# Kernel optimization log

Measured on AMD Instinct MI355X. Metric: run time of the kernel, lower is better.

Reference implementation:

```python
import jax, jax.numpy as jnp
import numpy as np

N_NODES, N_EDGES, N_FEAT, N_GRAPHS = 100_000, 1_600_000, 3, 512
FENG = jnp.array([4, 8, 9, 12, 13, 14])  # feng_filters(): second-order pairs with scale2 > scale1
LEAKY_SLOPE = 0.01


def _wavelet_constructor():
    # Psi_j = P^{2^{j-1}} - P^{2^j}, j = 1..4, over 17 diffusion levels P^0..P^16
    W = np.zeros((4, 17), dtype=np.float32)
    for j, (a, b) in enumerate([(1, 2), (2, 4), (4, 8), (8, 16)]):
        W[j, a] = 1.0
        W[j, b] = -1.0
    return jnp.asarray(W)


def _gcn_edges(edge_index, n):
    # gcn_norm with self-loops: w_ij = d_i^-1/2 d_j^-1/2 on A + I
    loop = jnp.arange(n)
    src = jnp.concatenate([edge_index[0], loop])
    dst = jnp.concatenate([edge_index[1], loop])
    deg = jax.ops.segment_sum(jnp.ones_like(dst, dtype=jnp.float32), dst, num_segments=n)
    dinv = jnp.where(deg > 0, jax.lax.rsqrt(deg), 0.0)
    w = dinv[src] * dinv[dst]
    return src, dst, w


def _diffuse(x, src, dst, w, n):
    # lazy random walk: 0.5 * (x + P_norm x), x: [N, C, k]
    agg = jax.ops.segment_sum(w[:, None, None] * x[src], dst, num_segments=n)
    return 0.5 * (x + agg)


def _scatter_features(x, edge_index):
    n, c = x.shape
    src, dst, w = _gcn_edges(edge_index, n)
    Wav = _wavelet_constructor()

    s0 = x[:, :, None]                                   # [N, C, 1]
    levels = [s0]
    for _ in range(16):
        levels.append(_diffuse(levels[-1], src, dst, w, n))
    D = jnp.stack(levels)                                # [17, N, C, 1]
    sub = jnp.einsum('wt,tnck->wnck', Wav, D)[..., 0]    # [4, N, C]
    s1 = jnp.abs(jnp.transpose(sub, (1, 2, 0)))          # [N, C, 4]

    levels2 = [s1]
    for _ in range(16):
        levels2.append(_diffuse(levels2[-1], src, dst, w, n))
    D2 = jnp.stack(levels2)                              # [17, N, C, 4]
    sub2 = jnp.einsum('wt,tncf->wncf', Wav, D2)          # [4, N, C, 4]
    # reproduce the exact torch transpose/reshape sequence of LEGS Scatter
    t = jnp.abs(jnp.transpose(sub2, (1, 0, 2, 3)).reshape(n, c, 16))  # [N, C, 16]
    s2 = jnp.swapaxes(t, 1, 2)[:, FENG]                  # [N, 6, C]

    xcat = jnp.concatenate([s0, s1], axis=2)             # [N, C, 5]
    xcat = jnp.swapaxes(xcat, 1, 2)                      # [N, 5, C]
    xcat = jnp.concatenate([xcat, s2], axis=1)           # [N, 11, C]
    return xcat.reshape(n, 11 * c)                       # [N, 33]


def _scatter_moments(x, batch, num_graphs):
    # per-graph mean / variance / skew (3 central moments), concatenated -> [G, 3*F]
    cnt = jax.ops.segment_sum(jnp.ones((x.shape[0],), x.dtype), batch, num_segments=num_graphs)
    cnt = jnp.maximum(cnt, 1.0)[:, None]
    mean = jax.ops.segment_sum(x, batch, num_segments=num_graphs) / cnt
    dev = x - mean[batch]
    var = jax.ops.segment_sum(dev * dev, batch, num_segments=num_graphs) / cnt
    skew = jax.ops.segment_sum(dev * dev * dev, batch, num_segments=num_graphs) / cnt
    return jnp.concatenate([mean, var, skew], axis=1)


def setup_inputs() -> dict:
    key = jax.random.key(0)
    ks = jax.random.split(key, 8)
    x = jax.random.normal(ks[0], (N_NODES, N_FEAT), dtype=jnp.float32)
    edge_index = jax.random.randint(ks[1], (2, N_EDGES), 0, N_NODES)
    batch = jnp.sort(jax.random.randint(ks[2], (N_NODES,), 0, N_GRAPHS))

    def lin(k, fan_in, fan_out):
        k1, k2 = jax.random.split(k)
        bound = 1.0 / np.sqrt(fan_in)
        W = jax.random.uniform(k1, (fan_in, fan_out), minval=-bound, maxval=bound, dtype=jnp.float32)
        b = jax.random.uniform(k2, (fan_out,), minval=-bound, maxval=bound, dtype=jnp.float32)
        return W, b

    W1, b1 = lin(ks[3], 99, 128)
    W2, b2 = lin(ks[4], 128, 64)
    W3, b3 = lin(ks[5], 64, 64)
    We, be = lin(ks[6], 64, 32)
    Wc, bc = lin(ks[7], 32, 1)
    return {"x": x, "W1": W1, "b1": b1, "W2": W2, "b2": b2, "W3": W3, "b3": b3,
            "We": We, "be": be, "Wc": Wc, "bc": bc,
            "edge_index": edge_index, "batch": batch, "num_graphs": N_GRAPHS}


def reference(x, W1, b1, W2, b2, W3, b3, We, be, Wc, bc, edge_index, batch, num_graphs):
    act = lambda v: jax.nn.leaky_relu(v, LEAKY_SLOPE)
    feats = _scatter_features(x, edge_index)              # [N, 33]
    h = _scatter_moments(feats, batch, num_graphs)        # [G, 99]
    h = act(h)
    h = act(h @ W1 + b1)        # dropout is identity (p=0.0)
    h = act(h @ W2 + b2)
    h = h @ W3 + b3             # no activation before embedding layer (as in source)
    embedding = h @ We + be
    output = embedding @ Wc + bc  # classifier applied to embedding (pre-activation)
    return embedding, output
```

## Files before the change

### kernel.cpp

```cpp
#include <hip/hip_runtime.h>

#define N_NODES 100000
#define N_EDGES 1600000
#define NG      512
#define NPART   8
#define NPP     12500
#define BCAP    245760
#define BQ      1024
#define BFLUSH  512
#define NBBLK   256
#define EPB     ((N_EDGES + NBBLK - 1) / NBBLK)
#define SCAT_SLICES 128

static __device__ __forceinline__ float lrelu(float v) {
    return v >= 0.0f ? v : 0.01f * v;
}

__global__ void k_zero_i32(int* __restrict__ p, int n) {
    int i = blockIdx.x * blockDim.x + threadIdx.x;
    if (i < n) p[i] = 0;
}

__global__ void k_copy_i32(const int* __restrict__ s, int* __restrict__ d, int n) {
    int i = blockIdx.x * blockDim.x + threadIdx.x;
    if (i < n) d[i] = s[i];
}

__global__ void k_dinv(const int* __restrict__ counts, float* __restrict__ dinv,
                       float* __restrict__ dinv2, float* __restrict__ sdeg) {
    int i = blockIdx.x * blockDim.x + threadIdx.x;
    if (i < N_NODES) {
        float deg = (float)(counts[i] + 1);
        float s = sqrtf(deg);
        sdeg[i] = s;
        dinv[i] = 1.0f / s;
        dinv2[i] = 1.0f / deg;
    }
}

__global__ __launch_bounds__(256) void k_bin(const int* __restrict__ esrc,
                                             const int* __restrict__ edst,
                                             int* __restrict__ gcur,
                                             uint2* __restrict__ gbuf) {
    __shared__ uint2 buf[NPART][BQ];
    __shared__ int lcnt[NPART];
    __shared__ int gbase[NPART];
    if (threadIdx.x < NPART) lcnt[threadIdx.x] = 0;
    __syncthreads();
    int base = blockIdx.x * EPB;
    int end = base + EPB; if (end > N_EDGES) end = N_EDGES;
    for (int r = base; r < end; r += 2048) {
        int rend = r + 2048; if (rend > end) rend = end;
        for (int e = r + (int)threadIdx.x; e < rend; e += 256) {
            int d = edst[e];
            int s = esrc[e];
            int b = d / NPP;
            int pos = atomicAdd(&lcnt[b], 1);
            if (pos < BQ) {
                buf[b][pos] = make_uint2((unsigned)s, (unsigned)d);
            } else {
                int g = atomicAdd(&gcur[b], 1);
                gbuf[(size_t)b * BCAP + g] = make_uint2((unsigned)s, (unsigned)d);
            }
        }
        __syncthreads();
        for (int b = 0; b < NPART; ++b) {
            int cnt = lcnt[b];
            if (cnt >= BFLUSH) {
                if (threadIdx.x == 0) gbase[b] = atomicAdd(&gcur[b], BFLUSH);
                __syncthreads();
                int gb = gbase[b];
                for (int i = threadIdx.x; i < BFLUSH; i += 256)
                    gbuf[(size_t)b * BCAP + gb + i] = buf[b][i];
                __syncthreads();
                int inb = cnt < BQ ? cnt : BQ;
                int rem = inb - BFLUSH;
                for (int i = threadIdx.x; i < rem; i += 256)
                    buf[b][i] = buf[b][BFLUSH + i];
                __syncthreads();
                if (threadIdx.x == 0) lcnt[b] = rem;
                __syncthreads();
            }
        }
    }
    for (int b = 0; b < NPART; ++b) {
        int cnt = lcnt[b]; if (cnt > BQ) cnt = BQ;
        if (cnt > 0) {
            if (threadIdx.x == 0) gbase[b] = atomicAdd(&gcur[b], cnt);
            __syncthreads();
            int gb = gbase[b];
            for (int i = threadIdx.x; i < cnt; i += 256)
                gbuf[(size_t)b * BCAP + gb + i] = buf[b][i];
        }
        __syncthreads();
    }
}

__global__ __launch_bounds__(1024) void k_count_b(const int* __restrict__ gcur,
                                                  const uint2* __restrict__ gbuf,
                                                  int* __restrict__ counts) {
    __shared__ int h[NPP];
    int p = blockIdx.x & (NPART - 1);
    int slice = blockIdx.x >> 3;
    for (int i = threadIdx.x; i < NPP; i += 1024) h[i] = 0;
    __syncthreads();
    int n = gcur[p];
    int per = (n + 7) / 8;
    int lo = slice * per, hi = lo + per; if (hi > n) hi = n;
    const uint2* bb = gbuf + (size_t)p * BCAP;
    int pl = p * NPP;
    for (int i = lo + (int)threadIdx.x; i < hi; i += 1024) {
        int d = (int)bb[i].y - pl;
        atomicAdd(&h[d], 1);
    }
    __syncthreads();
    for (int i = threadIdx.x; i < NPP; i += 1024)
        if (h[i]) atomicAdd(&counts[pl + i], h[i]);
}

__global__ void k_scan_block(const int* __restrict__ counts, int* __restrict__ offsets,
                             int* __restrict__ bsums, int n) {
    __shared__ int tmp[1024];
    int gid = blockIdx.x * 1024 + threadIdx.x;
    int v = (gid < n) ? counts[gid] : 0;
    tmp[threadIdx.x] = v;
    __syncthreads();
    for (int off = 1; off < 1024; off <<= 1) {
        int t = (threadIdx.x >= off) ? tmp[threadIdx.x - off] : 0;
        __syncthreads();
        tmp[threadIdx.x] += t;
        __syncthreads();
    }
    if (gid < n) offsets[gid + 1] = tmp[threadIdx.x];
    if (threadIdx.x == 1023) bsums[blockIdx.x] = tmp[1023];
}

__global__ void k_scan_bsums(int* __restrict__ bsums, int nb) {
    if (blockIdx.x == 0 && threadIdx.x == 0) {
        int acc = 0;
        for (int b = 0; b < nb; ++b) { int v = bsums[b]; bsums[b] = acc; acc += v; }
    }
}

__global__ void k_scan_add(int* __restrict__ offsets, const int* __restrict__ bsums, int n) {
    int gid = blockIdx.x * 1024 + threadIdx.x;
    if (gid < n) offsets[gid + 1] += bsums[blockIdx.x];
    if (gid == 0) offsets[0] = 0;
}

__global__ __launch_bounds__(256) void k_scatter_b(const int* __restrict__ gcur,
                                                   const uint2* __restrict__ gbuf,
                                                   int* __restrict__ cursor,
                                                   int* __restrict__ csr_src) {
    int p = blockIdx.x & (NPART - 1);
    int slice = blockIdx.x >> 3;
    int n = gcur[p];
    int per = (n + SCAT_SLICES - 1) / SCAT_SLICES;
    int lo = slice * per, hi = lo + per; if (hi > n) hi = n;
    const uint2* bb = gbuf + (size_t)p * BCAP;
    for (int i = lo + (int)threadIdx.x; i < hi; i += 256) {
        uint2 e = bb[i];
        int pos = atomicAdd(&cursor[e.y], 1);
        csr_src[pos] = (int)e.x;
    }
}

__global__ void k_vinit(const float* __restrict__ x, const float* __restrict__ dinv,
                        float4* __restrict__ v) {
    int i = blockIdx.x * blockDim.x + threadIdx.x;
    if (i >= N_NODES) return;
    float di = dinv[i];
    v[i] = make_float4(di * x[i * 3 + 0], di * x[i * 3 + 1], di * x[i * 3 + 2], 0.0f);
}

__global__ __launch_bounds__(256) void k_vdiff3(
    const float4* __restrict__ xin, float4* __restrict__ xout,
    const int* __restrict__ offs, const int* __restrict__ csrc,
    const float* __restrict__ dinv2) {
    int t = blockIdx.x * 256 + threadIdx.x;
    if (t >= N_NODES * 8) return;
    int h = t & 7;
    int i = t >> 3;
    int b = offs[i], e = offs[i + 1];
    float a0 = 0.0f, a1 = 0.0f, a2 = 0.0f;
    for (int p = b + h; p < e; p += 8) {
        int s = csrc[p];
        float4 xv = xin[s];
        a0 += xv.x; a1 += xv.y; a2 += xv.z;
    }
    a0 += __shfl_xor(a0, 1, 64); a1 += __shfl_xor(a1, 1, 64); a2 += __shfl_xor(a2, 1, 64);
    a0 += __shfl_xor(a0, 2, 64); a1 += __shfl_xor(a1, 2, 64); a2 += __shfl_xor(a2, 2, 64);
    a0 += __shfl_xor(a0, 4, 64); a1 += __shfl_xor(a1, 4, 64); a2 += __shfl_xor(a2, 4, 64);
    if (h == 0) {
        float d2 = dinv2[i];
        float4 sv = xin[i];
        xout[i] = make_float4(0.5f * (sv.x + d2 * (a0 + sv.x)),
                              0.5f * (sv.y + d2 * (a1 + sv.y)),
                              0.5f * (sv.z + d2 * (a2 + sv.z)), 0.0f);
    }
}

__global__ __launch_bounds__(256) void k_vdiff12(
    const float4* __restrict__ xin, float4* __restrict__ xout,
    const int* __restrict__ offs, const int* __restrict__ csrc,
    const float* __restrict__ dinv2) {
    int t = blockIdx.x * 256 + threadIdx.x;
    if (t >= N_NODES * 8) return;
    int h = t & 7;
    int i = t >> 3;
    int b = offs[i], e = offs[i + 1];
    float a[12];
#pragma unroll
    for (int c = 0; c < 12; ++c) a[c] = 0.0f;
    for (int p = b + h; p < e; p += 8) {
        int s = csrc[p];
        float4 b0 = xin[s * 3 + 0];
        float4 b1 = xin[s * 3 + 1];
        float4 b2 = xin[s * 3 + 2];
        a[0] += b0.x; a[1] += b0.y; a[2]  += b0.z; a[3]  += b0.w;
        a[4] += b1.x; a[5] += b1.y; a[6]  += b1.z; a[7]  += b1.w;
        a[8] += b2.x; a[9] += b2.y; a[10] += b2.z; a[11] += b2.w;
    }
#pragma unroll
    for (int c = 0; c < 12; ++c) {
        a[c] += __shfl_xor(a[c], 1, 64);
        a[c] += __shfl_xor(a[c], 2, 64);
        a[c] += __shfl_xor(a[c], 4, 64);
    }
    if (h == 0) {
        float d2 = dinv2[i];
        float4 s0 = xin[i * 3 + 0], s1 = xin[i * 3 + 1], s2 = xin[i * 3 + 2];
        xout[i * 3 + 0] = make_float4(0.5f * (s0.x + d2 * (a[0] + s0.x)),
                                      0.5f * (s0.y + d2 * (a[1] + s0.y)),
                                      0.5f * (s0.z + d2 * (a[2] + s0.z)),
                                      0.5f * (s0.w + d2 * (a[3] + s0.w)));
        xout[i * 3 + 1] = make_float4(0.5f * (s1.x + d2 * (a[4] + s1.x)),
                                      0.5f * (s1.y + d2 * (a[5] + s1.y)),
                                      0.5f * (s1.z + d2 * (a[6] + s1.z)),
                                      0.5f * (s1.w + d2 * (a[7] + s1.w)));
        xout[i * 3 + 2] = make_float4(0.5f * (s2.x + d2 * (a[8] + s2.x)),
                                      0.5f * (s2.y + d2 * (a[9] + s2.y)),
                                      0.5f * (s2.z + d2 * (a[10] + s2.z)),
                                      0.5f * (s2.w + d2 * (a[11] + s2.w)));
    }
}

__global__ void k_s1v(const float4* __restrict__ L1, const float4* __restrict__ L2,
                      const float4* __restrict__ L4, const float4* __restrict__ L8,
                      const float4* __restrict__ L16, float* __restrict__ s1v) {
    int i = blockIdx.x * blockDim.x + threadIdx.x;
    if (i >= N_NODES) return;
    float4 v[5];
    v[0] = L1[i]; v[1] = L2[i]; v[2] = L4[i]; v[3] = L8[i]; v[4] = L16[i];
    float* out = s1v + (size_t)i * 12;
#pragma unroll
    for (int f = 0; f < 4; ++f) {
        out[0 * 4 + f] = fabsf(v[f].x - v[f + 1].x);
        out[1 * 4 + f] = fabsf(v[f].y - v[f + 1].y);
        out[2 * 4 + f] = fabsf(v[f].z - v[f + 1].z);
    }
}

__global__ void k_feats(const float* __restrict__ x, const float* __restrict__ s1v,
                        const float* __restrict__ M1, const float* __restrict__ M2,
                        const float* __restrict__ M4, const float* __restrict__ M8,
                        const float* __restrict__ M16, const float* __restrict__ sdeg,
                        float* __restrict__ feats) {
    int i = blockIdx.x * blockDim.x + threadIdx.x;
    if (i >= N_NODES) return;
    float sd = sdeg[i];
    float* out = feats + (size_t)i * 33;
    out[0] = x[i * 3 + 0];
    out[1] = x[i * 3 + 1];
    out[2] = x[i * 3 + 2];
    for (int r = 1; r <= 4; ++r)
        for (int c = 0; c < 3; ++c)
            out[r * 3 + c] = sd * s1v[(size_t)i * 12 + c * 4 + (r - 1)];
    const float* Ms[5] = {M1, M2, M4, M8, M16};
    const int FENG[6] = {4, 8, 9, 12, 13, 14};
    for (int m = 0; m < 6; ++m) {
        for (int c2 = 0; c2 < 3; ++c2) {
            int idx = c2 * 16 + FENG[m];
            int w = idx / 12, rem = idx % 12, cc = rem / 4, f = rem % 4;
            float v = Ms[w][(size_t)i * 12 + cc * 4 + f] - Ms[w + 1][(size_t)i * 12 + cc * 4 + f];
            out[(5 + m) * 3 + c2] = fabsf(sd * v);
        }
    }
}

static __device__ __forceinline__ int lower_bound_i(const int* __restrict__ a, int n, int key) {
    int lo = 0, hi = n;
    while (lo < hi) { int mid = (lo + hi) >> 1; if (a[mid] < key) lo = mid + 1; else hi = mid; }
    return lo;
}

__global__ __launch_bounds__(256) void k_moments(
    const float* __restrict__ feats, const int* __restrict__ batch,
    float* __restrict__ h0) {
    __shared__ float P1[4][33], P2[4][33], P3[4][33];
    int g = blockIdx.x;
    int lo = lower_bound_i(batch, N_NODES, g);
    int hi = lower_bound_i(batch, N_NODES, g + 1);
    int w = threadIdx.x >> 6;
    int l = threadIdx.x & 63;
    float s1 = 0.0f, s2 = 0.0f, s3 = 0.0f;
    if (l < 33) {
        for (int i = lo + w; i < hi; i += 4) {
            float v = feats[(size_t)i * 33 + l];
            s1 += v;
            s2 += v * v;
            s3 += v * v * v;
        }
        P1[w][l] = s1; P2[w][l] = s2; P3[w][l] = s3;
    }
    __syncthreads();
    if (threadIdx.x < 33) {
        int c = threadIdx.x;
        float S1 = P1[0][c] + P1[1][c] + P1[2][c] + P1[3][c];
        float S2 = P2[0][c] + P2[1][c] + P2[2][c] + P2[3][c];
        float S3 = P3[0][c] + P3[1][c] + P3[2][c] + P3[3][c];
        float cnt = (float)((hi - lo) > 1 ? (hi - lo) : 1);
        float mu  = S1 / cnt;
        float ex2 = S2 / cnt;
        float ex3 = S3 / cnt;
        float var = ex2 - mu * mu;
        float skw = ex3 - 3.0f * mu * ex2 + 2.0f * mu * mu * mu;
        h0[g * 99 + c]      = lrelu(mu);
        h0[g * 99 + 33 + c] = lrelu(var);
        h0[g * 99 + 66 + c] = lrelu(skw);
    }
}

__global__ __launch_bounds__(128) void k_mlp(
    const float* __restrict__ h0,
    const float* __restrict__ W1, const float* __restrict__ b1,
    const float* __restrict__ W2, const float* __restrict__ b2,
    const float* __restrict__ W3, const float* __restrict__ b3,
    const float* __restrict__ We, const float* __restrict__ be,
    const float* __restrict__ Wc, const float* __restrict__ bc,
    float* __restrict__ emb, float* __restrict__ outp) {
    __shared__ float s0[99], s1[128], s2[64], s3[64], s4[32];
    int g = blockIdx.x;
    int t = threadIdx.x;
    if (t < 99) s0[t] = h0[g * 99 + t];
    __syncthreads();
    {
        float a = b1[t];
        for (int k = 0; k < 99; ++k) a += s0[k] * W1[k * 128 + t];
        s1[t] = lrelu(a);
    }
    __syncthreads();
    if (t < 64) {
        float a = b2[t];
        for (int k = 0; k < 128; ++k) a += s1[k] * W2[k * 64 + t];
        s2[t] = lrelu(a);
    }
    __syncthreads();
    if (t < 64) {
        float a = b3[t];
        for (int k = 0; k < 64; ++k) a += s2[k] * W3[k * 64 + t];
        s3[t] = a;
    }
    __syncthreads();
    if (t < 32) {
        float a = be[t];
        for (int k = 0; k < 64; ++k) a += s3[k] * We[k * 32 + t];
        s4[t] = a;
        emb[g * 32 + t] = a;
    }
    __syncthreads();
    if (t == 0) {
        float a = bc[0];
        for (int k = 0; k < 32; ++k) a += s4[k] * Wc[k];
        outp[g] = a;
    }
}

extern "C" void kernel_launch(void* const* d_in, const int* in_sizes, int n_in,
                              void* d_out, int out_size, void* d_ws, size_t ws_size,
                              hipStream_t stream) {
    const float* x   = (const float*)d_in[0];
    const float* W1  = (const float*)d_in[1];
    const float* b1  = (const float*)d_in[2];
    const float* W2  = (const float*)d_in[3];
    const float* b2  = (const float*)d_in[4];
    const float* W3  = (const float*)d_in[5];
    const float* b3  = (const float*)d_in[6];
    const float* We  = (const float*)d_in[7];
    const float* be  = (const float*)d_in[8];
    const float* Wc  = (const float*)d_in[9];
    const float* bc  = (const float*)d_in[10];
    const int*   eix = (const int*)d_in[11];
    const int*   batch = (const int*)d_in[12];
    const int* esrc = eix;
    const int* edst = eix + N_EDGES;

    char* ws = (char*)d_ws;
    size_t off = 0;
    auto alloc = [&](size_t bytes) -> void* {
        void* p = ws + off;
        off = (off + bytes + 255) & ~(size_t)255;
        return p;
    };
    int*   counts  = (int*)alloc((size_t)N_NODES * 4);
    int*   offsets = (int*)alloc((size_t)(N_NODES + 1) * 4);
    int*   cursor  = (int*)alloc((size_t)N_NODES * 4);
    float* dinv    = (float*)alloc((size_t)N_NODES * 4);
    float* dinv2   = (float*)alloc((size_t)N_NODES * 4);
    float* sdeg    = (float*)alloc((size_t)N_NODES * 4);
    int*   bsums   = (int*)alloc(1024 * 4);
    int*   gcur    = (int*)alloc(NPART * 4);
    uint2* gbuf    = (uint2*)alloc((size_t)NPART * BCAP * 8);
    int*   csr_src = (int*)alloc((size_t)N_EDGES * 4);
    float4* v0     = (float4*)alloc((size_t)N_NODES * 16);
    float4* p1[7];
    for (int i = 0; i < 7; ++i) p1[i] = (float4*)alloc((size_t)N_NODES * 16);
    float* s1v = (float*)alloc((size_t)N_NODES * 12 * 4);
    float* p2[7];
    for (int i = 0; i < 7; ++i) p2[i] = (float*)alloc((size_t)N_NODES * 12 * 4);
    float* feats = (float*)alloc((size_t)N_NODES * 33 * 4);
    float* h0 = (float*)alloc((size_t)NG * 99 * 4);
    (void)ws_size; (void)in_sizes; (void)n_in; (void)out_size;

    const int TB = 256;
    const int gbN = (N_NODES + TB - 1) / TB;
    const int nbScan = (N_NODES + 1023) / 1024;

    hipLaunchKernelGGL(k_zero_i32, dim3(gbN), dim3(TB), 0, stream, counts, N_NODES);
    hipLaunchKernelGGL(k_zero_i32, dim3(1), dim3(TB), 0, stream, gcur, NPART);
    hipLaunchKernelGGL(k_bin, dim3(NBBLK), dim3(TB), 0, stream, esrc, edst, gcur, gbuf);
    hipLaunchKernelGGL(k_count_b, dim3(64), dim3(1024), 0, stream, gcur, gbuf, counts);
    hipLaunchKernelGGL(k_dinv, dim3(gbN), dim3(TB), 0, stream, counts, dinv, dinv2, sdeg);
    hipLaunchKernelGGL(k_scan_block, dim3(nbScan), dim3(1024), 0, stream, counts, offsets, bsums, N_NODES);
    hipLaunchKernelGGL(k_scan_bsums, dim3(1), dim3(1), 0, stream, bsums, nbScan);
    hipLaunchKernelGGL(k_scan_add, dim3(nbScan), dim3(1024), 0, stream, offsets, bsums, N_NODES);
    hipLaunchKernelGGL(k_copy_i32, dim3(gbN), dim3(TB), 0, stream, offsets, cursor, N_NODES);
    hipLaunchKernelGGL(k_scatter_b, dim3(NPART * SCAT_SLICES), dim3(TB), 0, stream,
                       gcur, gbuf, cursor, csr_src);

    hipLaunchKernelGGL(k_vinit, dim3(gbN), dim3(TB), 0, stream, x, dinv, v0);

    const int saveT[5] = {1, 2, 4, 8, 16};

    const float4* prev = v0;
    float4* saves1[5];
    {
        int si = 0, sc = 0;
        const int gb = (N_NODES * 8 + TB - 1) / TB;
        for (int t = 1; t <= 16; ++t) {
            float4* outb;
            if (si < 5 && t == saveT[si]) { outb = p1[si]; saves1[si] = outb; ++si; }
            else { outb = p1[5 + sc]; sc ^= 1; }
            hipLaunchKernelGGL(k_vdiff3, dim3(gb), dim3(TB), 0, stream,
                               prev, outb, offsets, csr_src, dinv2);
            prev = outb;
        }
    }
    hipLaunchKernelGGL(k_s1v, dim3(gbN), dim3(TB), 0, stream,
                       saves1[0], saves1[1], saves1[2], saves1[3], saves1[4], s1v);

    float* saves2[5];
    {
        const float* prev2 = s1v;
        int si = 0, sc = 0;
        const int gb = (N_NODES * 8 + TB - 1) / TB;
        for (int t = 1; t <= 16; ++t) {
            float* outb;
            if (si < 5 && t == saveT[si]) { outb = p2[si]; saves2[si] = outb; ++si; }
            else { outb = p2[5 + sc]; sc ^= 1; }
            hipLaunchKernelGGL(k_vdiff12, dim3(gb), dim3(TB), 0, stream,
                               (const float4*)prev2, (float4*)outb, offsets, csr_src, dinv2);
            prev2 = outb;
        }
    }

    hipLaunchKernelGGL(k_feats, dim3(gbN), dim3(TB), 0, stream,
                       x, s1v, saves2[0], saves2[1], saves2[2], saves2[3], saves2[4], sdeg, feats);
    hipLaunchKernelGGL(k_moments, dim3(NG), dim3(256), 0, stream, feats, batch, h0);

    float* emb  = (float*)d_out;
    float* outp = (float*)d_out + NG * 32;
    hipLaunchKernelGGL(k_mlp, dim3(NG), dim3(128), 0, stream,
                       h0, W1, b1, W2, b2, W3, b3, We, be, Wc, bc, emb, outp);
}
```

Before: 809.4 us.

## Bin edges into 1024-node sub-ranges and pad second-order features to 16 floats

Replaces the 8-partition edge binning, global-atomic count and global-cursor scatter with 98 fine-grained bins of 1024 destination nodes. Each bin is then counted and placed into CSR with shared-memory histograms and cursors, staging the output in LDS. This removes the separate zero and copy passes and the global atomics on per-node cursors. Separately, the 12-float per-node vectors in the second-order diffusion are padded to 16 floats so each node's gather is 64-byte aligned. The cost is extra memory traffic for the padding and less parallelism during placement, since only 98 blocks run.

```diff
diff --git a/kernel.cpp b/kernel.cpp
--- a/kernel.cpp
+++ b/kernel.cpp
@@ -3,14 +3,13 @@
 #define N_NODES 100000
 #define N_EDGES 1600000
 #define NG      512
-#define NPART   8
-#define NPP     12500
-#define BCAP    245760
-#define BQ      1024
-#define BFLUSH  512
-#define NBBLK   256
-#define EPB     ((N_EDGES + NBBLK - 1) / NBBLK)
-#define SCAT_SLICES 128
+#define NSB     98
+#define SUBR    1024
+#define SCAP    20480
+#define SD      96
+#define B2BLK   256
+#define B2E     ((N_EDGES + B2BLK - 1) / B2BLK)
+#define PCAP    18432
 
 static __device__ __forceinline__ float lrelu(float v) {
     return v >= 0.0f ? v : 0.01f * v;
@@ -19,11 +18,6 @@
 __global__ void k_zero_i32(int* __restrict__ p, int n) {
     int i = blockIdx.x * blockDim.x + threadIdx.x;
     if (i < n) p[i] = 0;
-}
-
-__global__ void k_copy_i32(const int* __restrict__ s, int* __restrict__ d, int n) {
-    int i = blockIdx.x * blockDim.x + threadIdx.x;
-    if (i < n) d[i] = s[i];
 }
 
 __global__ void k_dinv(const int* __restrict__ counts, float* __restrict__ dinv,
@@ -38,84 +32,59 @@
     }
 }
 
-__global__ __launch_bounds__(256) void k_bin(const int* __restrict__ esrc,
-                                             const int* __restrict__ edst,
-                                             int* __restrict__ gcur,
-                                             uint2* __restrict__ gbuf) {
-    __shared__ uint2 buf[NPART][BQ];
-    __shared__ int lcnt[NPART];
-    __shared__ int gbase[NPART];
-    if (threadIdx.x < NPART) lcnt[threadIdx.x] = 0;
-    __syncthreads();
-    int base = blockIdx.x * EPB;
-    int end = base + EPB; if (end > N_EDGES) end = N_EDGES;
-    for (int r = base; r < end; r += 2048) {
-        int rend = r + 2048; if (rend > end) rend = end;
-        for (int e = r + (int)threadIdx.x; e < rend; e += 256) {
-            int d = edst[e];
-            int s = esrc[e];
-            int b = d / NPP;
-            int pos = atomicAdd(&lcnt[b], 1);
-            if (pos < BQ) {
-                buf[b][pos] = make_uint2((unsigned)s, (unsigned)d);
-            } else {
-                int g = atomicAdd(&gcur[b], 1);
-                gbuf[(size_t)b * BCAP + g] = make_uint2((unsigned)s, (unsigned)d);
-            }
+__global__ __launch_bounds__(256) void k_bin2(const int* __restrict__ esrc,
+                                              const int* __restrict__ edst,
+                                              int* __restrict__ gcur,
+                                              uint2* __restrict__ gbuf) {
+    __shared__ uint2 st[NSB][SD];
+    __shared__ int lcnt[NSB];
+    __shared__ int gbase[NSB];
+    for (int i = threadIdx.x; i < NSB; i += 256) lcnt[i] = 0;
+    __syncthreads();
+    int base = blockIdx.x * B2E;
+    int end = base + B2E; if (end > N_EDGES) end = N_EDGES;
+    for (int e = base + (int)threadIdx.x; e < end; e += 256) {
+        int d = edst[e];
+        int s = esrc[e];
+        int b = d >> 10;
+        int pos = atomicAdd(&lcnt[b], 1);
+        if (pos < SD) {
+            st[b][pos] = make_uint2((unsigned)s, (unsigned)d);
+        } else {
+            int g = atomicAdd(&gcur[b], 1);
+            gbuf[(size_t)b * SCAP + g] = make_uint2((unsigned)s, (unsigned)d);
         }
-        __syncthreads();
-        for (int b = 0; b < NPART; ++b) {
-            int cnt = lcnt[b];
-            if (cnt >= BFLUSH) {
-                if (threadIdx.x == 0) gbase[b] = atomicAdd(&gcur[b], BFLUSH);
-                __syncthreads();
-                int gb = gbase[b];
-                for (int i = threadIdx.x; i < BFLUSH; i += 256)
-                    gbuf[(size_t)b * BCAP + gb + i] = buf[b][i];
-                __syncthreads();
-                int inb = cnt < BQ ? cnt : BQ;
-                int rem = inb - BFLUSH;
-                for (int i = threadIdx.x; i < rem; i += 256)
-                    buf[b][i] = buf[b][BFLUSH + i];
-                __syncthreads();
-                if (threadIdx.x == 0) lcnt[b] = rem;
-                __syncthreads();
-            }
-        }
-    }
-    for (int b = 0; b < NPART; ++b) {
-        int cnt = lcnt[b]; if (cnt > BQ) cnt = BQ;
-        if (cnt > 0) {
-            if (threadIdx.x == 0) gbase[b] = atomicAdd(&gcur[b], cnt);
-            __syncthreads();
-            int gb = gbase[b];
-            for (int i = threadIdx.x; i < cnt; i += 256)
-                gbuf[(size_t)b * BCAP + gb + i] = buf[b][i];
-        }
-        __syncthreads();
-    }
-}
-
-__global__ __launch_bounds__(1024) void k_count_b(const int* __restrict__ gcur,
-                                                  const uint2* __restrict__ gbuf,
-                                                  int* __restrict__ counts) {
-    __shared__ int h[NPP];
-    int p = blockIdx.x & (NPART - 1);
-    int slice = blockIdx.x >> 3;
-    for (int i = threadIdx.x; i < NPP; i += 1024) h[i] = 0;
-    __syncthreads();
-    int n = gcur[p];
-    int per = (n + 7) / 8;
-    int lo = slice * per, hi = lo + per; if (hi > n) hi = n;
-    const uint2* bb = gbuf + (size_t)p * BCAP;
-    int pl = p * NPP;
-    for (int i = lo + (int)threadIdx.x; i < hi; i += 1024) {
-        int d = (int)bb[i].y - pl;
-        atomicAdd(&h[d], 1);
-    }
-    __syncthreads();
-    for (int i = threadIdx.x; i < NPP; i += 1024)
-        if (h[i]) atomicAdd(&counts[pl + i], h[i]);
+    }
+    __syncthreads();
+    if (threadIdx.x < NSB) {
+        int c = lcnt[threadIdx.x]; if (c > SD) c = SD;
+        gbase[threadIdx.x] = atomicAdd(&gcur[threadIdx.x], c);
+    }
+    __syncthreads();
+    for (int b = 0; b < NSB; ++b) {
+        int cnt = lcnt[b]; if (cnt > SD) cnt = SD;
+        int gb = gbase[b];
+        for (int i = threadIdx.x; i < cnt; i += 256)
+            gbuf[(size_t)b * SCAP + gb + i] = st[b][i];
+    }
+}
+
+__global__ __launch_bounds__(256) void k_count_s(const int* __restrict__ gcur,
+                                                 const uint2* __restrict__ gbuf,
+                                                 int* __restrict__ counts) {
+    __shared__ int h[SUBR];
+    int sb = blockIdx.x;
+    int lo = sb * SUBR;
+    int nr = N_NODES - lo; if (nr > SUBR) nr = SUBR;
+    for (int i = threadIdx.x; i < nr; i += 256) h[i] = 0;
+    __syncthreads();
+    int n = gcur[sb];
+    const uint2* bb = gbuf + (size_t)sb * SCAP;
+    for (int i = threadIdx.x; i < n; i += 256)
+        atomicAdd(&h[(int)bb[i].y - lo], 1);
+    __syncthreads();
+    for (int i = threadIdx.x; i < nr; i += 256)
+        counts[lo + i] = h[i];
 }
 
 __global__ void k_scan_block(const int* __restrict__ counts, int* __restrict__ offsets,
@@ -148,21 +117,32 @@
     if (gid == 0) offsets[0] = 0;
 }
 
-__global__ __launch_bounds__(256) void k_scatter_b(const int* __restrict__ gcur,
-                                                   const uint2* __restrict__ gbuf,
-                                                   int* __restrict__ cursor,
-                                                   int* __restrict__ csr_src) {
-    int p = blockIdx.x & (NPART - 1);
-    int slice = blockIdx.x >> 3;
-    int n = gcur[p];
-    int per = (n + SCAT_SLICES - 1) / SCAT_SLICES;
-    int lo = slice * per, hi = lo + per; if (hi > n) hi = n;
-    const uint2* bb = gbuf + (size_t)p * BCAP;
-    for (int i = lo + (int)threadIdx.x; i < hi; i += 256) {
+__global__ __launch_bounds__(256) void k_place(const int* __restrict__ gcur,
+                                               const uint2* __restrict__ gbuf,
+                                               const int* __restrict__ offsets,
+                                               int* __restrict__ csr_src) {
+    __shared__ int cur[SUBR];
+    __shared__ int stage[PCAP];
+    int sb = blockIdx.x;
+    int lo = sb * SUBR;
+    int nr = N_NODES - lo; if (nr > SUBR) nr = SUBR;
+    int base = offsets[lo];
+    int total = offsets[lo + nr] - base;
+    for (int i = threadIdx.x; i < nr; i += 256)
+        cur[i] = offsets[lo + i] - base;
+    __syncthreads();
+    int n = gcur[sb];
+    const uint2* bb = gbuf + (size_t)sb * SCAP;
+    for (int i = threadIdx.x; i < n; i += 256) {
         uint2 e = bb[i];
-        int pos = atomicAdd(&cursor[e.y], 1);
-        csr_src[pos] = (int)e.x;
-    }
+        int p = atomicAdd(&cur[(int)e.y - lo], 1);
+        if (p < PCAP) stage[p] = (int)e.x;
+        else csr_src[base + p] = (int)e.x;
+    }
+    __syncthreads();
+    int wtot = total < PCAP ? total : PCAP;
+    for (int i = threadIdx.x; i < wtot; i += 256)
+        csr_src[base + i] = stage[i];
 }
 
 __global__ void k_vinit(const float* __restrict__ x, const float* __restrict__ dinv,
@@ -214,9 +194,9 @@
     for (int c = 0; c < 12; ++c) a[c] = 0.0f;
     for (int p = b + h; p < e; p += 8) {
         int s = csrc[p];
-        float4 b0 = xin[s * 3 + 0];
-        float4 b1 = xin[s * 3 + 1];
-        float4 b2 = xin[s * 3 + 2];
+        float4 b0 = xin[s * 4 + 0];
+        float4 b1 = xin[s * 4 + 1];
+        float4 b2 = xin[s * 4 + 2];
         a[0] += b0.x; a[1] += b0.y; a[2]  += b0.z; a[3]  += b0.w;
         a[4] += b1.x; a[5] += b1.y; a[6]  += b1.z; a[7]  += b1.w;
         a[8] += b2.x; a[9] += b2.y; a[10] += b2.z; a[11] += b2.w;
@@ -229,16 +209,16 @@
     }
     if (h == 0) {
         float d2 = dinv2[i];
-        float4 s0 = xin[i * 3 + 0], s1 = xin[i * 3 + 1], s2 = xin[i * 3 + 2];
-        xout[i * 3 + 0] = make_float4(0.5f * (s0.x + d2 * (a[0] + s0.x)),
+        float4 s0 = xin[i * 4 + 0], s1 = xin[i * 4 + 1], s2 = xin[i * 4 + 2];
+        xout[i * 4 + 0] = make_float4(0.5f * (s0.x + d2 * (a[0] + s0.x)),
                                       0.5f * (s0.y + d2 * (a[1] + s0.y)),
                                       0.5f * (s0.z + d2 * (a[2] + s0.z)),
                                       0.5f * (s0.w + d2 * (a[3] + s0.w)));
-        xout[i * 3 + 1] = make_float4(0.5f * (s1.x + d2 * (a[4] + s1.x)),
+        xout[i * 4 + 1] = make_float4(0.5f * (s1.x + d2 * (a[4] + s1.x)),
                                       0.5f * (s1.y + d2 * (a[5] + s1.y)),
                                       0.5f * (s1.z + d2 * (a[6] + s1.z)),
                                       0.5f * (s1.w + d2 * (a[7] + s1.w)));
-        xout[i * 3 + 2] = make_float4(0.5f * (s2.x + d2 * (a[8] + s2.x)),
+        xout[i * 4 + 2] = make_float4(0.5f * (s2.x + d2 * (a[8] + s2.x)),
                                       0.5f * (s2.y + d2 * (a[9] + s2.y)),
                                       0.5f * (s2.z + d2 * (a[10] + s2.z)),
                                       0.5f * (s2.w + d2 * (a[11] + s2.w)));
@@ -247,12 +227,12 @@
 
 __global__ void k_s1v(const float4* __restrict__ L1, const float4* __restrict__ L2,
                       const float4* __restrict__ L4, const float4* __restrict__ L8,
-                      const float4* __restrict__ L16, float* __restrict__ s1v) {
+                      const float4* __restrict__ L16, float* __restrict__ s1vp) {
     int i = blockIdx.x * blockDim.x + threadIdx.x;
     if (i >= N_NODES) return;
     float4 v[5];
     v[0] = L1[i]; v[1] = L2[i]; v[2] = L4[i]; v[3] = L8[i]; v[4] = L16[i];
-    float* out = s1v + (size_t)i * 12;
+    float* out = s1vp + (size_t)i * 16;
 #pragma unroll
     for (int f = 0; f < 4; ++f) {
         out[0 * 4 + f] = fabsf(v[f].x - v[f + 1].x);
@@ -261,7 +241,7 @@
     }
 }
 
-__global__ void k_feats(const float* __restrict__ x, const float* __restrict__ s1v,
+__global__ void k_feats(const float* __restrict__ x, const float* __restrict__ s1vp,
                         const float* __restrict__ M1, const float* __restrict__ M2,
                         const float* __restrict__ M4, const float* __restrict__ M8,
                         const float* __restrict__ M16, const float* __restrict__ sdeg,
@@ -275,14 +255,14 @@
     out[2] = x[i * 3 + 2];
     for (int r = 1; r <= 4; ++r)
         for (int c = 0; c < 3; ++c)
-            out[r * 3 + c] = sd * s1v[(size_t)i * 12 + c * 4 + (r - 1)];
+            out[r * 3 + c] = sd * s1vp[(size_t)i * 16 + c * 4 + (r - 1)];
     const float* Ms[5] = {M1, M2, M4, M8, M16};
     const int FENG[6] = {4, 8, 9, 12, 13, 14};
     for (int m = 0; m < 6; ++m) {
         for (int c2 = 0; c2 < 3; ++c2) {
             int idx = c2 * 16 + FENG[m];
             int w = idx / 12, rem = idx % 12, cc = rem / 4, f = rem % 4;
-            float v = Ms[w][(size_t)i * 12 + cc * 4 + f] - Ms[w + 1][(size_t)i * 12 + cc * 4 + f];
+            float v = Ms[w][(size_t)i * 16 + cc * 4 + f] - Ms[w + 1][(size_t)i * 16 + cc * 4 + f];
             out[(5 + m) * 3 + c2] = fabsf(sd * v);
         }
     }
@@ -404,20 +384,19 @@
     };
     int*   counts  = (int*)alloc((size_t)N_NODES * 4);
     int*   offsets = (int*)alloc((size_t)(N_NODES + 1) * 4);
-    int*   cursor  = (int*)alloc((size_t)N_NODES * 4);
     float* dinv    = (float*)alloc((size_t)N_NODES * 4);
     float* dinv2   = (float*)alloc((size_t)N_NODES * 4);
     float* sdeg    = (float*)alloc((size_t)N_NODES * 4);
     int*   bsums   = (int*)alloc(1024 * 4);
-    int*   gcur    = (int*)alloc(NPART * 4);
-    uint2* gbuf    = (uint2*)alloc((size_t)NPART * BCAP * 8);
+    int*   gcur    = (int*)alloc(NSB * 4);
+    uint2* gbuf    = (uint2*)alloc((size_t)NSB * SCAP * 8);
     int*   csr_src = (int*)alloc((size_t)N_EDGES * 4);
     float4* v0     = (float4*)alloc((size_t)N_NODES * 16);
     float4* p1[7];
     for (int i = 0; i < 7; ++i) p1[i] = (float4*)alloc((size_t)N_NODES * 16);
-    float* s1v = (float*)alloc((size_t)N_NODES * 12 * 4);
+    float* s1vp = (float*)alloc((size_t)N_NODES * 16 * 4);
     float* p2[7];
-    for (int i = 0; i < 7; ++i) p2[i] = (float*)alloc((size_t)N_NODES * 12 * 4);
+    for (int i = 0; i < 7; ++i) p2[i] = (float*)alloc((size_t)N_NODES * 16 * 4);
     float* feats = (float*)alloc((size_t)N_NODES * 33 * 4);
     float* h0 = (float*)alloc((size_t)NG * 99 * 4);
     (void)ws_size; (void)in_sizes; (void)n_in; (void)out_size;
@@ -426,17 +405,14 @@
     const int gbN = (N_NODES + TB - 1) / TB;
     const int nbScan = (N_NODES + 1023) / 1024;
 
-    hipLaunchKernelGGL(k_zero_i32, dim3(gbN), dim3(TB), 0, stream, counts, N_NODES);
-    hipLaunchKernelGGL(k_zero_i32, dim3(1), dim3(TB), 0, stream, gcur, NPART);
-    hipLaunchKernelGGL(k_bin, dim3(NBBLK), dim3(TB), 0, stream, esrc, edst, gcur, gbuf);
-    hipLaunchKernelGGL(k_count_b, dim3(64), dim3(1024), 0, stream, gcur, gbuf, counts);
+    hipLaunchKernelGGL(k_zero_i32, dim3(1), dim3(TB), 0, stream, gcur, NSB);
+    hipLaunchKernelGGL(k_bin2, dim3(B2BLK), dim3(TB), 0, stream, esrc, edst, gcur, gbuf);
+    hipLaunchKernelGGL(k_count_s, dim3(NSB), dim3(TB), 0, stream, gcur, gbuf, counts);
     hipLaunchKernelGGL(k_dinv, dim3(gbN), dim3(TB), 0, stream, counts, dinv, dinv2, sdeg);
     hipLaunchKernelGGL(k_scan_block, dim3(nbScan), dim3(1024), 0, stream, counts, offsets, bsums, N_NODES);
     hipLaunchKernelGGL(k_scan_bsums, dim3(1), dim3(1), 0, stream, bsums, nbScan);
     hipLaunchKernelGGL(k_scan_add, dim3(nbScan), dim3(1024), 0, stream, offsets, bsums, N_NODES);
-    hipLaunchKernelGGL(k_copy_i32, dim3(gbN), dim3(TB), 0, stream, offsets, cursor, N_NODES);
-    hipLaunchKernelGGL(k_scatter_b, dim3(NPART * SCAT_SLICES), dim3(TB), 0, stream,
-                       gcur, gbuf, cursor, csr_src);
+    hipLaunchKernelGGL(k_place, dim3(NSB), dim3(TB), 0, stream, gcur, gbuf, offsets, csr_src);
 
     hipLaunchKernelGGL(k_vinit, dim3(gbN), dim3(TB), 0, stream, x, dinv, v0);
 
@@ -457,11 +433,11 @@
         }
     }
     hipLaunchKernelGGL(k_s1v, dim3(gbN), dim3(TB), 0, stream,
-                       saves1[0], saves1[1], saves1[2], saves1[3], saves1[4], s1v);
+                       saves1[0], saves1[1], saves1[2], saves1[3], saves1[4], s1vp);
 
     float* saves2[5];
     {
-        const float* prev2 = s1v;
+        const float* prev2 = s1vp;
         int si = 0, sc = 0;
         const int gb = (N_NODES * 8 + TB - 1) / TB;
         for (int t = 1; t <= 16; ++t) {
@@ -475,7 +451,7 @@
     }
 
     hipLaunchKernelGGL(k_feats, dim3(gbN), dim3(TB), 0, stream,
-                       x, s1v, saves2[0], saves2[1], saves2[2], saves2[3], saves2[4], sdeg, feats);
+                       x, s1vp, saves2[0], saves2[1], saves2[2], saves2[3], saves2[4], sdeg, feats);
     hipLaunchKernelGGL(k_moments, dim3(NG), dim3(256), 0, stream, feats, batch, h0);
 
     float* emb  = (float*)d_out;
```

Result: faster. 746.8 us (-7.7%).
